# Performance work log

Measured on AMD Instinct MI355X. Metric: run time of the kernel, lower is better.

The kernel has to match this reference:

```python
import jax, jax.numpy as jnp
import numpy as np

PF = 8
BITS = 4
T, D, O, A = 1024, 2048, 4096, 4  # tokens, in_dim, per-slice out_dim, max_deltas


def _dequant(qw, qz, sc):
    """GPTQ-style 4-bit dequant, single quant group (g_idx all zero).
    qw: [O, D//PF] int32 (nibbles packed along input dim)
    qz: [O//PF, 1] int32 (zero nibbles packed along output dim)
    sc: [O, 1] float scales
    returns W: [O, D] float32
    """
    Od, Kp = qw.shape
    shifts = jnp.arange(PF, dtype=jnp.int32) * BITS
    q = ((qw[:, :, None] >> shifts) & 0xF).reshape(Od, Kp * PF).astype(jnp.float32)
    z = ((qz[:, 0][:, None] >> shifts) & 0xF).reshape(Od)[:, None].astype(jnp.float32)
    return sc.astype(jnp.float32) * (q - z)


def _delta_slice(x, indices, qw_s, qz_s, sc_s):
    # per-token adapter dispatch: tokens with indices==a use delta weight a
    out = jnp.zeros((x.shape[0], qw_s.shape[1]), dtype=jnp.float32)
    for a in range(qw_s.shape[0]):  # fixed small loop over adapters
        W = _dequant(qw_s[a], qz_s[a], sc_s[a])           # [O, D]
        xm = jnp.where((indices == a)[:, None], x, 0.0)    # gather-by-mask
        out = out + xm @ W.T                               # [T, O]
    return out


def setup_inputs() -> dict:
    key = jax.random.key(0)
    ks = jax.random.split(key, 10)
    MAXI = np.int32(2147483647)
    return {
        "x": jax.random.normal(ks[0], (T, D), dtype=jnp.float32),
        "base_weight": jax.random.normal(ks[1], (2 * O, D), dtype=jnp.float32) * 0.02,
        "base_bias": jax.random.normal(ks[2], (2 * O,), dtype=jnp.float32) * 0.02,
        "qweight_0": jax.random.randint(ks[3], (A, O, D // PF), 0, MAXI, dtype=jnp.int32),
        "qweight_1": jax.random.randint(ks[4], (A, O, D // PF), 0, MAXI, dtype=jnp.int32),
        "qzeros_0": jax.random.randint(ks[5], (A, O // PF, 1), 0, MAXI, dtype=jnp.int32),
        "qzeros_1": jax.random.randint(ks[6], (A, O // PF, 1), 0, MAXI, dtype=jnp.int32),
        "scales_0": jax.random.uniform(ks[7], (A, O, 1), dtype=jnp.float32) * 1e-3,
        "scales_1": jax.random.uniform(ks[8], (A, O, 1), dtype=jnp.float32) * 1e-3,
        "g_idx_0": jnp.zeros((D,), dtype=jnp.int32),
        "g_idx_1": jnp.zeros((D,), dtype=jnp.int32),
        "indices": jax.random.randint(ks[9], (T,), 0, A, dtype=jnp.int32),
    }


def reference(x, base_weight, base_bias, qweight_0, qweight_1, qzeros_0, qzeros_1,
              scales_0, scales_1, g_idx_0, g_idx_1, indices):
    # base ColumnParallelLinear GEMM (+bias, skip_bias_add=False)
    out = x @ base_weight.T + base_bias  # [T, 2*O]
    # apply_delta_packed_nslice onto the two equal output slices
    d0 = _delta_slice(x, indices, qweight_0, qzeros_0, scales_0)
    d1 = _delta_slice(x, indices, qweight_1, qzeros_1, scales_1)
    return out + jnp.concatenate([d0, d1], axis=1)
```

## Files before the change

### kernel.cpp

```cpp
#include <hip/hip_runtime.h>
#include <stdint.h>

#define T_TOK 1024
#define DIN   2048
#define NOUT  8192
#define OSL   4096
#define ROWS_PAD 1408
#define BM 128
#define BN 128
#define BK 32
#define NT (DIN / BK)
#define BUF1 16384

typedef _Float16 f16x8 __attribute__((ext_vector_type(8)));
typedef _Float16 f16x2 __attribute__((ext_vector_type(2)));
typedef float    f32x4 __attribute__((ext_vector_type(4)));

__device__ __forceinline__ void gload16(const void* gp, void* lp) {
  __builtin_amdgcn_global_load_lds(
      (__attribute__((address_space(1))) void*)gp,
      (__attribute__((address_space(3))) void*)lp, 16, 0, 0);
}

__device__ __forceinline__ f16x2 u2h(uint32_t u) {
  union { uint32_t u; f16x2 h; } c; c.u = u; return c.h;
}

__device__ __forceinline__ f16x8 cvt_interleave(float4 f0, float4 f1) {
  f16x8 h;
  h[0] = (_Float16)f0.x; h[1] = (_Float16)f1.x;
  h[2] = (_Float16)f0.y; h[3] = (_Float16)f1.y;
  h[4] = (_Float16)f0.z; h[5] = (_Float16)f1.z;
  h[6] = (_Float16)f0.w; h[7] = (_Float16)f1.w;
  return h;
}

#define VMCNT5() asm volatile("s_waitcnt vmcnt(5)" ::: "memory")
#define VMCNT0() asm volatile("s_waitcnt vmcnt(0)" ::: "memory")
#define LGKM0()  asm volatile("s_waitcnt lgkmcnt(0)" ::: "memory")

__global__ void prep(const float* __restrict__ x, const float* __restrict__ wb,
                     const int* __restrict__ indices,
                     _Float16* __restrict__ xh, _Float16* __restrict__ wbh,
                     int* __restrict__ inv, int* __restrict__ meta)
{
  const int b = blockIdx.x;
  const int tid = threadIdx.x;

  if (b == 0) {
    __shared__ int cnt[4], cur[4];
    if (tid < 4) cnt[tid] = 0;
    __syncthreads();
    for (int t = tid; t < T_TOK; t += 256) atomicAdd(&cnt[indices[t]], 1);
    __syncthreads();
    if (tid == 0) {
      int off = 0;
      for (int a = 0; a < 4; ++a) {
        meta[a] = off;
        meta[5 + a] = off + cnt[a];
        cur[a] = off;
        off = (off + cnt[a] + 127) & ~127;
      }
      meta[4] = off;
    }
    __syncthreads();
    for (int i = tid; i < ROWS_PAD; i += 256) inv[i] = -1;
    __syncthreads();
    for (int t = tid; t < T_TOK; t += 256) {
      int a = indices[t];
      int p = atomicAdd(&cur[a], 1);
      inv[p] = t;
    }
    return;
  }

  if (b <= 1 + T_TOK) {
    const int row = b - 1;
    const int d0 = tid * 8;
    f16x8 h;
    if (row < T_TOK) {
      const float* src = x + (size_t)row * DIN + d0;
      h = cvt_interleave(*(const float4*)src, *(const float4*)(src + 4));
    } else {
#pragma unroll
      for (int j = 0; j < 8; ++j) h[j] = (_Float16)0.0f;
    }
    *(f16x8*)(xh + (size_t)row * DIN + d0) = h;
    return;
  }

  const int n = b - (2 + T_TOK);
  const int d0 = tid * 8;
  const float* src = wb + (size_t)n * DIN + d0;
  f16x8 v = cvt_interleave(*(const float4*)src, *(const float4*)(src + 4));
  *(f16x8*)(wbh + (size_t)n * DIN + d0) = v;
}

__global__ __launch_bounds__(256) void kfuse(
    const _Float16* __restrict__ xh, const _Float16* __restrict__ wbh,
    const int* __restrict__ qw0, const int* __restrict__ qw1,
    const int* __restrict__ qz0, const int* __restrict__ qz1,
    const float* __restrict__ sc0, const float* __restrict__ sc1,
    const float* __restrict__ bias,
    const int* __restrict__ inv, const int* __restrict__ meta,
    float* __restrict__ out)
{
  const int id = blockIdx.y * 64 + blockIdx.x;
  const int m0 = (id >> 6) * BM;
  const int n0 = (((id & 7) << 3) | ((id >> 3) & 7)) * BN;

  if (m0 >= meta[4]) return;
  int ad = 0;
  if (m0 >= meta[1]) ad = 1;
  if (m0 >= meta[2]) ad = 2;
  if (m0 >= meta[3]) ad = 3;
  if (m0 >= meta[5 + ad]) return;

  const int sl = n0 >> 12;
  const int tid  = threadIdx.x;
  const int wave = tid >> 6;
  const int lane = tid & 63;
  const int quad = lane >> 4;
  const int l16  = lane & 15;
  const int wm = (wave & 1) << 6;
  const int wn = (wave >> 1) << 6;

  __shared__ __align__(16) char smem[32768];

  f32x4 acc[4][4];
#pragma unroll
  for (int i = 0; i < 4; ++i)
#pragma unroll
    for (int j = 0; j < 4; ++j) acc[i][j] = (f32x4)0.0f;

  const int kch = (((tid & 3) ^ ((tid >> 3) & 3)) << 3);
  const int rloc = tid >> 2;
  int r0 = inv[m0 + rloc];       if (r0 < 0) r0 = T_TOK;
  int r1 = inv[m0 + rloc + 64];  if (r1 < 0) r1 = T_TOK;
  const _Float16* ag0 = xh + (size_t)r0 * DIN + kch;
  const _Float16* ag1 = xh + (size_t)r1 * DIN + kch;
  const int saoff0 = wave * 1024;
  const int saoff1 = 4096 + wave * 1024;

  const int o_local = tid >> 1;
  const int o = n0 + o_local;
  const int o_sl = o & (OSL - 1);
  const int* qwp = (sl ? qw1 : qw0) + ((size_t)ad * OSL + o_sl) * (DIN / 8) + ((tid & 1) << 1);
  const int zw = (sl ? qz1 : qz0)[ad * (OSL / 8) + (o_sl >> 3)];
  const float s = (sl ? sc1 : sc0)[(size_t)ad * OSL + o_sl];
  const int z = (zw >> ((o_sl & 7) << 2)) & 0xF;
  f16x2 s2; s2[0] = s2[1] = (_Float16)s;
  f16x2 k2; k2[0] = k2[1] = (_Float16)(float)(-(1024 + z));
  const _Float16* wbp = wbh + (size_t)o * DIN + ((tid & 1) << 4);

  const int bswz = (o_local >> 1) & 3;
  const int bwoff0 = 8192 + o_local * 64 + (((((tid & 1) << 1)    ) ^ bswz) << 4);
  const int bwoff1 = 8192 + o_local * 64 + (((((tid & 1) << 1) | 1) ^ bswz) << 4);
  const int qoff = ((quad ^ ((l16 >> 1) & 3)) << 4);

  auto LOADREGS = [&](int t, int2 &qv, f16x8 &wa, f16x8 &wb2) {
    qv  = *(const int2*)(qwp + t * 4);
    wa  = *(const f16x8*)(wbp + t * BK);
    wb2 = *(const f16x8*)(wbp + t * BK + 8);
  };
  auto GLOADS = [&](int bb, int t) {
    gload16(ag0 + t * BK, smem + bb + saoff0);
    gload16(ag1 + t * BK, smem + bb + saoff1);
  };
  auto DEQW = [&](int bb, int2 qv, f16x8 wa, f16x8 wb2) {
    const uint32_t wx = (uint32_t)qv.x, wy = (uint32_t)qv.y;
    union U { f16x8 v; f16x2 p[4]; } A_, B_, h0, h1;
    A_.v = wa; B_.v = wb2;
#pragma unroll
    for (int j = 0; j < 4; ++j) {
      uint32_t t0 = ((wx >> (4 * j)) & 0x000F000Fu) | 0x64006400u;
      uint32_t t1 = ((wy >> (4 * j)) & 0x000F000Fu) | 0x64006400u;
      h0.p[j] = (u2h(t0) + k2) * s2 + A_.p[j];
      h1.p[j] = (u2h(t1) + k2) * s2 + B_.p[j];
    }
    *(f16x8*)(smem + bb + bwoff0) = h0.v;
    *(f16x8*)(smem + bb + bwoff1) = h1.v;
  };
  auto COMPUTE = [&](int bb) {
    f16x8 af[4], bf[4];
#pragma unroll
    for (int t = 0; t < 4; ++t)
      af[t] = *(const f16x8*)(smem + bb + (wm + t * 16 + l16) * 64 + qoff);
#pragma unroll
    for (int t = 0; t < 4; ++t)
      bf[t] = *(const f16x8*)(smem + bb + 8192 + (wn + t * 16 + l16) * 64 + qoff);
    __builtin_amdgcn_s_setprio(1);
#pragma unroll
    for (int mt = 0; mt < 4; ++mt)
#pragma unroll
      for (int nt = 0; nt < 4; ++nt)
        acc[mt][nt] = __builtin_amdgcn_mfma_f32_16x16x32_f16(af[mt], bf[nt], acc[mt][nt], 0, 0, 0);
    __builtin_amdgcn_s_setprio(0);
  };

  int2 qvA, qvB;
  f16x8 waA, wbA2, waB, wbB2;

  LOADREGS(0, qvA, waA, wbA2);
  GLOADS(0, 0);
  LOADREGS(1, qvB, waB, wbB2);
  GLOADS(BUF1, 1);
  VMCNT5();
  __builtin_amdgcn_sched_barrier(0);
  DEQW(0, qvA, waA, wbA2);
  LGKM0();
  __builtin_amdgcn_s_barrier();

  for (int t = 0; t < NT - 2; t += 2) {
    LOADREGS(t + 2, qvA, waA, wbA2);
    COMPUTE(0);
    __builtin_amdgcn_s_barrier();
    __builtin_amdgcn_sched_barrier(0);
    GLOADS(0, t + 2);
    VMCNT5();
    __builtin_amdgcn_sched_barrier(0);
    DEQW(BUF1, qvB, waB, wbB2);
    LGKM0();
    __builtin_amdgcn_s_barrier();

    LOADREGS(t + 3, qvB, waB, wbB2);
    COMPUTE(BUF1);
    __builtin_amdgcn_s_barrier();
    __builtin_amdgcn_sched_barrier(0);
    GLOADS(BUF1, t + 3);
    VMCNT5();
    __builtin_amdgcn_sched_barrier(0);
    DEQW(0, qvA, waA, wbA2);
    LGKM0();
    __builtin_amdgcn_s_barrier();
  }

  COMPUTE(0);
  VMCNT0();
  __builtin_amdgcn_sched_barrier(0);
  DEQW(BUF1, qvB, waB, wbB2);
  LGKM0();
  __builtin_amdgcn_s_barrier();
  COMPUTE(BUF1);

#pragma unroll
  for (int mt = 0; mt < 4; ++mt) {
    const int rowb = m0 + wm + mt * 16 + quad * 4;
    int tk[4];
#pragma unroll
    for (int r = 0; r < 4; ++r) tk[r] = inv[rowb + r];
#pragma unroll
    for (int nt = 0; nt < 4; ++nt) {
      const int col = n0 + wn + nt * 16 + l16;
      const float bv = bias[col];
#pragma unroll
      for (int r = 0; r < 4; ++r) {
        if (tk[r] >= 0)
          out[(size_t)tk[r] * NOUT + col] = acc[mt][nt][r] + bv;
      }
    }
  }
}

extern "C" void kernel_launch(void* const* d_in, const int* in_sizes, int n_in,
                              void* d_out, int out_size, void* d_ws, size_t ws_size,
                              hipStream_t stream) {
  const float* x    = (const float*)d_in[0];
  const float* wb   = (const float*)d_in[1];
  const float* bias = (const float*)d_in[2];
  const int*   qw0  = (const int*)d_in[3];
  const int*   qw1  = (const int*)d_in[4];
  const int*   qz0  = (const int*)d_in[5];
  const int*   qz1  = (const int*)d_in[6];
  const float* sc0  = (const float*)d_in[7];
  const float* sc1  = (const float*)d_in[8];
  const int*   indices = (const int*)d_in[11];
  float* out = (float*)d_out;

  char* w = (char*)d_ws;
  _Float16* xh = (_Float16*)w;
  size_t off = (size_t)(T_TOK + 1) * DIN * 2;
  int* inv  = (int*)(w + off);
  int* meta = inv + ROWS_PAD;
  size_t woff = (off + (size_t)ROWS_PAD * 4 + 64 + 255) & ~(size_t)255;
  _Float16* wbh = (_Float16*)(w + woff);

  prep<<<2 + T_TOK + NOUT, 256, 0, stream>>>(x, wb, indices, xh, wbh, inv, meta);
  kfuse<<<dim3(64, 11), 256, 0, stream>>>(xh, wbh, qw0, qw1, qz0, qz1, sc0, sc1,
                                          bias, inv, meta, out);
}
```

Measured before the change: 247.0 us.

## Fuse base-weight fp32-to-fp16 conversion into GEMM and restructure pipeline

Drops the separate prep pass that converted the fp32 base weight to fp16 in a workspace buffer. The fused kernel now loads fp32 base weight directly and converts it during the dequant/add step. The main loop is also rewritten into a single-barrier-per-iteration schedule that issues the next A-tile load, loads registers, computes and dequantizes in one step. This removes a 64MB read plus 32MB write/read round trip, at the cost of doubling base-weight bytes read per GEMM tile, since each tile is re-read across the M blocks, and more register pressure from the fp32 staging.

```diff
diff --git a/kernel.cpp b/kernel.cpp
--- a/kernel.cpp
+++ b/kernel.cpp
@@ -38,11 +38,11 @@
 #define VMCNT5() asm volatile("s_waitcnt vmcnt(5)" ::: "memory")
 #define VMCNT0() asm volatile("s_waitcnt vmcnt(0)" ::: "memory")
 #define LGKM0()  asm volatile("s_waitcnt lgkmcnt(0)" ::: "memory")
-
-__global__ void prep(const float* __restrict__ x, const float* __restrict__ wb,
-                     const int* __restrict__ indices,
-                     _Float16* __restrict__ xh, _Float16* __restrict__ wbh,
-                     int* __restrict__ inv, int* __restrict__ meta)
+#define SB0()    __builtin_amdgcn_sched_barrier(0)
+
+__global__ void prep(const float* __restrict__ x, const int* __restrict__ indices,
+                     _Float16* __restrict__ xh, int* __restrict__ inv,
+                     int* __restrict__ meta)
 {
   const int b = blockIdx.x;
   const int tid = threadIdx.x;
@@ -74,30 +74,21 @@
     return;
   }
 
-  if (b <= 1 + T_TOK) {
-    const int row = b - 1;
-    const int d0 = tid * 8;
-    f16x8 h;
-    if (row < T_TOK) {
-      const float* src = x + (size_t)row * DIN + d0;
-      h = cvt_interleave(*(const float4*)src, *(const float4*)(src + 4));
-    } else {
-#pragma unroll
-      for (int j = 0; j < 8; ++j) h[j] = (_Float16)0.0f;
-    }
-    *(f16x8*)(xh + (size_t)row * DIN + d0) = h;
-    return;
-  }
-
-  const int n = b - (2 + T_TOK);
+  const int row = b - 1;
   const int d0 = tid * 8;
-  const float* src = wb + (size_t)n * DIN + d0;
-  f16x8 v = cvt_interleave(*(const float4*)src, *(const float4*)(src + 4));
-  *(f16x8*)(wbh + (size_t)n * DIN + d0) = v;
+  f16x8 h;
+  if (row < T_TOK) {
+    const float* src = x + (size_t)row * DIN + d0;
+    h = cvt_interleave(*(const float4*)src, *(const float4*)(src + 4));
+  } else {
+#pragma unroll
+    for (int j = 0; j < 8; ++j) h[j] = (_Float16)0.0f;
+  }
+  *(f16x8*)(xh + (size_t)row * DIN + d0) = h;
 }
 
 __global__ __launch_bounds__(256) void kfuse(
-    const _Float16* __restrict__ xh, const _Float16* __restrict__ wbh,
+    const _Float16* __restrict__ xh, const float* __restrict__ wbf32,
     const int* __restrict__ qw0, const int* __restrict__ qw1,
     const int* __restrict__ qz0, const int* __restrict__ qz1,
     const float* __restrict__ sc0, const float* __restrict__ sc1,
@@ -151,26 +142,25 @@
   const int z = (zw >> ((o_sl & 7) << 2)) & 0xF;
   f16x2 s2; s2[0] = s2[1] = (_Float16)s;
   f16x2 k2; k2[0] = k2[1] = (_Float16)(float)(-(1024 + z));
-  const _Float16* wbp = wbh + (size_t)o * DIN + ((tid & 1) << 4);
+  const float* wbp = wbf32 + (size_t)o * DIN + ((tid & 1) << 4);
 
   const int bswz = (o_local >> 1) & 3;
   const int bwoff0 = 8192 + o_local * 64 + (((((tid & 1) << 1)    ) ^ bswz) << 4);
   const int bwoff1 = 8192 + o_local * 64 + (((((tid & 1) << 1) | 1) ^ bswz) << 4);
   const int qoff = ((quad ^ ((l16 >> 1) & 3)) << 4);
 
-  auto LOADREGS = [&](int t, int2 &qv, f16x8 &wa, f16x8 &wb2) {
-    qv  = *(const int2*)(qwp + t * 4);
-    wa  = *(const f16x8*)(wbp + t * BK);
-    wb2 = *(const f16x8*)(wbp + t * BK + 8);
-  };
-  auto GLOADS = [&](int bb, int t) {
-    gload16(ag0 + t * BK, smem + bb + saoff0);
-    gload16(ag1 + t * BK, smem + bb + saoff1);
-  };
-  auto DEQW = [&](int bb, int2 qv, f16x8 wa, f16x8 wb2) {
+  auto LOADREGS = [&](int t, int2& qv, float4* f) {
+    qv   = *(const int2*)(qwp + t * 4);
+    f[0] = *(const float4*)(wbp + t * BK);
+    f[1] = *(const float4*)(wbp + t * BK + 4);
+    f[2] = *(const float4*)(wbp + t * BK + 8);
+    f[3] = *(const float4*)(wbp + t * BK + 12);
+  };
+  auto DEQW = [&](int bb, int2 qv, const float4* f) {
+    union U { f16x8 v; f16x2 p[4]; } A_, B_, h0, h1;
+    A_.v = cvt_interleave(f[0], f[1]);
+    B_.v = cvt_interleave(f[2], f[3]);
     const uint32_t wx = (uint32_t)qv.x, wy = (uint32_t)qv.y;
-    union U { f16x8 v; f16x2 p[4]; } A_, B_, h0, h1;
-    A_.v = wa; B_.v = wb2;
 #pragma unroll
     for (int j = 0; j < 4; ++j) {
       uint32_t t0 = ((wx >> (4 * j)) & 0x000F000Fu) | 0x64006400u;
@@ -199,48 +189,42 @@
   };
 
   int2 qvA, qvB;
-  f16x8 waA, wbA2, waB, wbB2;
-
-  LOADREGS(0, qvA, waA, wbA2);
-  GLOADS(0, 0);
-  LOADREGS(1, qvB, waB, wbB2);
-  GLOADS(BUF1, 1);
-  VMCNT5();
-  __builtin_amdgcn_sched_barrier(0);
-  DEQW(0, qvA, waA, wbA2);
+  float4 fA[4], fB[4];
+
+  LOADREGS(0, qvB, fB);
+  gload16(ag0, smem + saoff0);
+  gload16(ag1, smem + saoff1);
+  VMCNT0(); SB0();
+  DEQW(0, qvB, fB);
+  LOADREGS(1, qvA, fA);
   LGKM0();
-  __builtin_amdgcn_s_barrier();
-
-  for (int t = 0; t < NT - 2; t += 2) {
-    LOADREGS(t + 2, qvA, waA, wbA2);
-    COMPUTE(0);
-    __builtin_amdgcn_s_barrier();
-    __builtin_amdgcn_sched_barrier(0);
-    GLOADS(0, t + 2);
-    VMCNT5();
-    __builtin_amdgcn_sched_barrier(0);
-    DEQW(BUF1, qvB, waB, wbB2);
+  __builtin_amdgcn_s_barrier(); SB0();
+
+  auto ITER_FULL = [&](int bb_cur, int bb_nxt, int t, int2& qvP, float4* fP,
+                       int2& qvN, float4* fN) {
+    gload16(ag0 + (t + 1) * BK, smem + bb_nxt + saoff0);
+    gload16(ag1 + (t + 1) * BK, smem + bb_nxt + saoff1);
+    SB0();
+    LOADREGS(t + 2, qvN, fN);
+    COMPUTE(bb_cur);
+    DEQW(bb_nxt, qvP, fP);
+    SB0(); VMCNT5(); SB0();
     LGKM0();
-    __builtin_amdgcn_s_barrier();
-
-    LOADREGS(t + 3, qvB, waB, wbB2);
-    COMPUTE(BUF1);
-    __builtin_amdgcn_s_barrier();
-    __builtin_amdgcn_sched_barrier(0);
-    GLOADS(BUF1, t + 3);
-    VMCNT5();
-    __builtin_amdgcn_sched_barrier(0);
-    DEQW(0, qvA, waA, wbA2);
-    LGKM0();
-    __builtin_amdgcn_s_barrier();
-  }
-
+    __builtin_amdgcn_s_barrier(); SB0();
+  };
+
+  for (int t = 0; t < NT - 4; t += 2) {
+    ITER_FULL(0, BUF1, t,     qvA, fA, qvB, fB);
+    ITER_FULL(BUF1, 0, t + 1, qvB, fB, qvA, fA);
+  }
+  ITER_FULL(0, BUF1, NT - 4, qvA, fA, qvB, fB);
+  ITER_FULL(BUF1, 0, NT - 3, qvB, fB, qvA, fA);
+  gload16(ag0 + (NT - 1) * BK, smem + BUF1 + saoff0);
+  gload16(ag1 + (NT - 1) * BK, smem + BUF1 + saoff1);
   COMPUTE(0);
-  VMCNT0();
-  __builtin_amdgcn_sched_barrier(0);
-  DEQW(BUF1, qvB, waB, wbB2);
-  LGKM0();
-  __builtin_amdgcn_s_barrier();
+  DEQW(BUF1, qvA, fA);
+  SB0(); VMCNT0(); SB0(); LGKM0();
+  __builtin_amdgcn_s_barrier(); SB0();
   COMPUTE(BUF1);
 
 #pragma unroll
@@ -282,10 +266,8 @@
   size_t off = (size_t)(T_TOK + 1) * DIN * 2;
   int* inv  = (int*)(w + off);
   int* meta = inv + ROWS_PAD;
-  size_t woff = (off + (size_t)ROWS_PAD * 4 + 64 + 255) & ~(size_t)255;
-  _Float16* wbh = (_Float16*)(w + woff);
-
-  prep<<<2 + T_TOK + NOUT, 256, 0, stream>>>(x, wb, indices, xh, wbh, inv, meta);
-  kfuse<<<dim3(64, 11), 256, 0, stream>>>(xh, wbh, qw0, qw1, qz0, qz1, sc0, sc1,
+
+  prep<<<2 + T_TOK, 256, 0, stream>>>(x, indices, xh, inv, meta);
+  kfuse<<<dim3(64, 11), 256, 0, stream>>>(xh, wb, qw0, qw1, qz0, qz1, sc0, sc1,
                                           bias, inv, meta, out);
 }
```

Result: slower. 274.5 us (+11.2%).
